# Kernel tuning notes

Hardware: AMD Instinct MI355X
Metric: run time of the kernel (lower is better)

Reference implementation:

```python
import jax, jax.numpy as jnp
import numpy as np

B, N, D, H, O, K, N_USER, C = 1, 4096, 64, 4, 64, 2, 4000, 2


def setup_inputs() -> dict:
    key = jax.random.key(0)
    ks = jax.random.split(key, 7)
    h = jax.random.normal(ks[0], (B, N, D), jnp.float32)
    # dense 0/1 adjacency per heterogeneous kind, with self-loops so no row is empty
    adj = jax.random.randint(ks[1], (K, B, N, N), 0, 2).astype(jnp.float32)
    hadj = jnp.maximum(adj, jnp.eye(N, dtype=jnp.float32))
    s = 1.0 / np.sqrt(D).astype(np.float32)
    w = jax.random.normal(ks[2], (K, H, D, O), jnp.float32) * s
    a_src = jax.random.normal(ks[3], (K, H, O, 1), jnp.float32) * (1.0 / np.sqrt(O).astype(np.float32))
    a_dst = jax.random.normal(ks[4], (K, H, O, 1), jnp.float32) * (1.0 / np.sqrt(O).astype(np.float32))
    fc_w = jax.random.normal(ks[5], (C, O * K), jnp.float32) * (1.0 / np.sqrt(O * K).astype(np.float32))
    fc_b = jnp.zeros((C,), jnp.float32)
    return {"h": h, "hadj": hadj, "w": w, "a_src": a_src, "a_dst": a_dst, "fc_w": fc_w, "fc_b": fc_b}


def _gat(h, adj, w_k, a_src_k, a_dst_k):
    # h: (B,N,D); adj: (B,N,N); w_k: (H,D,O); a_*: (H,O,1)
    h_prime = jnp.einsum('bnf,hfo->bhno', h, w_k)          # (B,H,N,O)
    t = jnp.tanh(h_prime)
    attn_src = jnp.einsum('bhno,hoi->bhni', t, a_src_k)    # (B,H,N,1)
    attn_dst = jnp.einsum('bhno,hoi->bhni', t, a_dst_k)    # (B,H,N,1)
    attn = attn_src + jnp.swapaxes(attn_dst, -1, -2)       # (B,H,N,N) broadcast add
    attn = jnp.where(attn >= 0, attn, 0.2 * attn)          # LeakyReLU(0.2)
    attn = jnp.where(adj[:, None] > 0, attn, -jnp.inf)     # dense mask
    attn = jax.nn.softmax(attn, axis=-1)                   # dropout is a no-op in eval
    out = jnp.einsum('bhnm,bhmo->bhno', attn, h_prime)     # (B,H,N,O)
    return out.mean(axis=1)                                # mean over heads -> (B,N,O)


def reference(h, hadj, w, a_src, a_dst, fc_w, fc_b):
    embs = []
    for k in range(K):  # small fixed loop over heterogeneous node kinds
        x = _gat(h, hadj[k], w[k], a_src[k], a_dst[k])
        embs.append(x[:, :N_USER])
    type_aware = jnp.concatenate(embs, axis=-1)            # (B, N_USER, K*O)
    logits = type_aware @ fc_w.T + fc_b                    # (B, N_USER, C)
    return jax.nn.log_softmax(logits, axis=-1)
```

## Files before the change

### kernel.cpp

```cpp
#include <hip/hip_runtime.h>
#include <math.h>

constexpr int KK = 2;
constexpr int HH = 4;
constexpr int NN = 4096;
constexpr int DD = 64;
constexpr int OO = 64;
constexpr int NU = 4000;
constexpr int CC = 2;
constexpr float LOG2E = 1.44269504088896340736f;

typedef float vf4 __attribute__((ext_vector_type(4)));
typedef float vf2 __attribute__((ext_vector_type(2)));

__device__ __forceinline__ float fexp2(float x) {
#if __has_builtin(__builtin_amdgcn_exp2f)
  return __builtin_amdgcn_exp2f(x);
#else
  return exp2f(x);
#endif
}
__device__ __forceinline__ float frcp(float x) {
#if __has_builtin(__builtin_amdgcn_rcpf)
  return __builtin_amdgcn_rcpf(x);
#else
  return 1.0f / x;
#endif
}
__device__ __forceinline__ float ftanh(float x) {
  float e = fexp2(x * (2.0f * LOG2E));
  return 1.0f - 2.0f * frcp(e + 1.0f);
}

__global__ __launch_bounds__(256) void gat_phase1(
    const float* __restrict__ hsrc, const float* __restrict__ w,
    const float* __restrict__ a_src, const float* __restrict__ a_dst,
    const float* __restrict__ fc_w,
    float* __restrict__ srcAA, float* __restrict__ Bp,
    float* __restrict__ B5p, float* __restrict__ g0p,
    float* __restrict__ g1p) {
  const int kh = blockIdx.y;
  const int k = kh >> 2;
  const int i0 = blockIdx.x * 64;
  const int tid = threadIdx.x;

  __shared__ float h_s[DD][68];
  __shared__ float w_s[DD][OO];
  __shared__ float part[4][64][17];

  {
    const vf4* wp = (const vf4*)(w + (size_t)kh * DD * OO);
    vf4* ws4 = (vf4*)w_s;
    for (int t = tid; t < DD * OO / 4; t += 256) ws4[t] = wp[t];
  }
  for (int t = tid; t < 1024; t += 256) {
    const int row = t >> 4;
    const int f4 = (t & 15) * 4;
    vf4 v = *(const vf4*)(hsrc + (size_t)(i0 + row) * DD + f4);
    h_s[f4 + 0][row] = v.x;
    h_s[f4 + 1][row] = v.y;
    h_s[f4 + 2][row] = v.z;
    h_s[f4 + 3][row] = v.w;
  }
  __syncthreads();

  const int og = tid & 15;
  const int rg = tid >> 4;
  const int o0 = og * 4;
  const int r0 = rg * 4;

  float hp[4][4];
#pragma unroll
  for (int j = 0; j < 4; ++j)
#pragma unroll
    for (int u = 0; u < 4; ++u) hp[j][u] = 0.0f;

#pragma unroll 8
  for (int f = 0; f < DD; ++f) {
    vf4 hv = *(const vf4*)&h_s[f][r0];
    vf4 wv = *(const vf4*)&w_s[f][o0];
    hp[0][0] = fmaf(hv.x, wv.x, hp[0][0]);
    hp[0][1] = fmaf(hv.x, wv.y, hp[0][1]);
    hp[0][2] = fmaf(hv.x, wv.z, hp[0][2]);
    hp[0][3] = fmaf(hv.x, wv.w, hp[0][3]);
    hp[1][0] = fmaf(hv.y, wv.x, hp[1][0]);
    hp[1][1] = fmaf(hv.y, wv.y, hp[1][1]);
    hp[1][2] = fmaf(hv.y, wv.z, hp[1][2]);
    hp[1][3] = fmaf(hv.y, wv.w, hp[1][3]);
    hp[2][0] = fmaf(hv.z, wv.x, hp[2][0]);
    hp[2][1] = fmaf(hv.z, wv.y, hp[2][1]);
    hp[2][2] = fmaf(hv.z, wv.z, hp[2][2]);
    hp[2][3] = fmaf(hv.z, wv.w, hp[2][3]);
    hp[3][0] = fmaf(hv.w, wv.x, hp[3][0]);
    hp[3][1] = fmaf(hv.w, wv.y, hp[3][1]);
    hp[3][2] = fmaf(hv.w, wv.z, hp[3][2]);
    hp[3][3] = fmaf(hv.w, wv.w, hp[3][3]);
  }

  float as[4], ad[4], f0[4], f1[4];
#pragma unroll
  for (int u = 0; u < 4; ++u) {
    as[u] = a_src[kh * OO + o0 + u];
    ad[u] = a_dst[kh * OO + o0 + u];
    f0[u] = fc_w[0 * (KK * OO) + k * OO + o0 + u];
    f1[u] = fc_w[1 * (KK * OO) + k * OO + o0 + u];
  }

#pragma unroll
  for (int j = 0; j < 4; ++j) {
    float sp = 0.0f, dp = 0.0f, g0 = 0.0f, g1 = 0.0f;
#pragma unroll
    for (int u = 0; u < 4; ++u) {
      float v = hp[j][u];
      float t = ftanh(v);
      sp = fmaf(t, as[u], sp);
      dp = fmaf(t, ad[u], dp);
      g0 = fmaf(v, f0[u], g0);
      g1 = fmaf(v, f1[u], g1);
    }
    part[0][r0 + j][og] = sp;
    part[1][r0 + j][og] = dp;
    part[2][r0 + j][og] = g0;
    part[3][r0 + j][og] = g1;
  }
  __syncthreads();

  {
    const int val = tid & 3;
    const int j2 = tid >> 2;
    const float* pr = &part[val][j2][0];
    vf4 s0 = *(const vf4*)(pr + 0);
    vf4 s1 = *(const vf4*)(pr + 4);
    vf4 s2 = *(const vf4*)(pr + 8);
    vf4 s3 = *(const vf4*)(pr + 12);
    vf4 t4 = s0 + s1 + s2 + s3;
    float sum = t4.x + t4.y + t4.z + t4.w;
    const size_t idx = (size_t)kh * NN + i0 + j2;
    if (val == 0) {
      float sp = sum * LOG2E;
      vf2 v = {fexp2(sp), fexp2(0.2f * sp)};
      *(vf2*)(srcAA + idx * 2) = v;
    } else if (val == 1) {
      float dp = sum * LOG2E;
      Bp[idx] = fexp2(dp);
      B5p[idx] = fexp2(0.2f * dp);
    } else if (val == 2) {
      g0p[idx] = sum;
    } else {
      g1p[idx] = sum;
    }
  }
}

__global__ __launch_bounds__(256) void gat_phase2(
    const float* __restrict__ adj, const float* __restrict__ srcAA,
    const float* __restrict__ Bp, const float* __restrict__ B5p,
    const float* __restrict__ g0p, const float* __restrict__ g1p,
    float* __restrict__ S) {
  const int k = blockIdx.y;
  const int r0 = blockIdx.x * 4;
  const int tid = threadIdx.x;
  const int wave = tid >> 6;
  const int lane = tid & 63;

  float A[4][4], A5[4][4];
#pragma unroll
  for (int h = 0; h < 4; ++h) {
    const float* base = srcAA + ((size_t)(k * HH + h) * NN + r0) * 2;
#pragma unroll
    for (int r = 0; r < 4; ++r) {
      A[r][h] = base[r * 2 + 0];
      A5[r][h] = base[r * 2 + 1];
    }
  }

  vf2 l2[4][4], a02[4][4], a12[4][4];
#pragma unroll
  for (int r = 0; r < 4; ++r)
#pragma unroll
    for (int h = 0; h < 4; ++h) {
      l2[r][h] = (vf2)(0.0f);
      a02[r][h] = (vf2)(0.0f);
      a12[r][h] = (vf2)(0.0f);
    }

  const float* adjk = adj + (size_t)k * NN * NN;
  const int jw = wave * 1024 + lane * 4;

#pragma unroll 1
  for (int t = 0; t < 4; ++t) {
    const int j = jw + t * 256;
    vf4 av[4];
#pragma unroll
    for (int r = 0; r < 4; ++r)
      av[r] = *(const vf4*)(adjk + (size_t)(r0 + r) * NN + j);
#pragma unroll
    for (int h = 0; h < 4; ++h) {
      const size_t pb = (size_t)(k * HH + h) * NN + j;
      vf4 b = *(const vf4*)(Bp + pb);
      vf4 b5 = *(const vf4*)(B5p + pb);
      vf4 g0 = *(const vf4*)(g0p + pb);
      vf4 g1 = *(const vf4*)(g1p + pb);
      vf2 blo = {b.x, b.y}, bhi = {b.z, b.w};
      vf2 b5lo = {b5.x, b5.y}, b5hi = {b5.z, b5.w};
      vf2 g0lo = {g0.x, g0.y}, g0hi = {g0.z, g0.w};
      vf2 g1lo = {g1.x, g1.y}, g1hi = {g1.z, g1.w};
#pragma unroll
      for (int r = 0; r < 4; ++r) {
        vf2 alo = {av[r].x, av[r].y}, ahi = {av[r].z, av[r].w};
        {
          vf2 e = __builtin_elementwise_max(blo * A[r][h], b5lo * A5[r][h]);
          vf2 pa = e * alo;
          l2[r][h] += pa;
          a02[r][h] = __builtin_elementwise_fma(pa, g0lo, a02[r][h]);
          a12[r][h] = __builtin_elementwise_fma(pa, g1lo, a12[r][h]);
        }
        {
          vf2 e = __builtin_elementwise_max(bhi * A[r][h], b5hi * A5[r][h]);
          vf2 pa = e * ahi;
          l2[r][h] += pa;
          a02[r][h] = __builtin_elementwise_fma(pa, g0hi, a02[r][h]);
          a12[r][h] = __builtin_elementwise_fma(pa, g1hi, a12[r][h]);
        }
      }
    }
  }

  float red[4][4][3];
#pragma unroll
  for (int r = 0; r < 4; ++r)
#pragma unroll
    for (int h = 0; h < 4; ++h) {
      float x0 = l2[r][h].x + l2[r][h].y;
      float x1 = a02[r][h].x + a02[r][h].y;
      float x2 = a12[r][h].x + a12[r][h].y;
#pragma unroll
      for (int off = 32; off > 0; off >>= 1) {
        x0 += __shfl_xor(x0, off, 64);
        x1 += __shfl_xor(x1, off, 64);
        x2 += __shfl_xor(x2, off, 64);
      }
      red[r][h][0] = x0;
      red[r][h][1] = x1;
      red[r][h][2] = x2;
    }

  __shared__ float sred[4][48];
  if (lane == 0) {
#pragma unroll
    for (int r = 0; r < 4; ++r)
#pragma unroll
      for (int h = 0; h < 4; ++h) {
#pragma unroll
        for (int c = 0; c < 3; ++c)
          sred[wave][(r * 4 + h) * 3 + c] = red[r][h][c];
      }
  }
  __syncthreads();
  if (tid < 8) {
    const int r = tid >> 1, c = tid & 1;
    float acc = 0.0f;
#pragma unroll
    for (int h = 0; h < 4; ++h) {
      const int vb = (r * 4 + h) * 3;
      float ls = sred[0][vb] + sred[1][vb] + sred[2][vb] + sred[3][vb];
      float ac = sred[0][vb + 1 + c] + sred[1][vb + 1 + c] +
                 sred[2][vb + 1 + c] + sred[3][vb + 1 + c];
      acc += ac / ls;
    }
    S[((size_t)k * NU + r0 + r) * CC + c] = 0.25f * acc;
  }
}

__global__ __launch_bounds__(256) void gat_phase3(
    const float* __restrict__ S, const float* __restrict__ fc_b,
    float* __restrict__ out) {
  const int i = blockIdx.x * 256 + threadIdx.x;
  if (i >= NU) return;
  float l0 = S[(size_t)i * CC + 0] + S[((size_t)NU + i) * CC + 0] + fc_b[0];
  float l1 = S[(size_t)i * CC + 1] + S[((size_t)NU + i) * CC + 1] + fc_b[1];
  float m = fmaxf(l0, l1);
  float lse = m + logf(expf(l0 - m) + expf(l1 - m));
  out[i * CC + 0] = l0 - lse;
  out[i * CC + 1] = l1 - lse;
}

extern "C" void kernel_launch(void* const* d_in, const int* in_sizes, int n_in,
                              void* d_out, int out_size, void* d_ws, size_t ws_size,
                              hipStream_t stream) {
  const float* hsrc  = (const float*)d_in[0];
  const float* hadj  = (const float*)d_in[1];
  const float* w     = (const float*)d_in[2];
  const float* a_src = (const float*)d_in[3];
  const float* a_dst = (const float*)d_in[4];
  const float* fc_w  = (const float*)d_in[5];
  const float* fc_b  = (const float*)d_in[6];
  float* out = (float*)d_out;

  char* ws = (char*)d_ws;
  float* srcAA = (float*)(ws + 0);
  float* Bp    = (float*)(ws + 262144);
  float* B5p   = (float*)(ws + 393216);
  float* g0p   = (float*)(ws + 524288);
  float* g1p   = (float*)(ws + 655360);
  float* S     = (float*)(ws + 786432);

  dim3 g1(NN / 64, KK * HH);
  gat_phase1<<<g1, 256, 0, stream>>>(hsrc, w, a_src, a_dst, fc_w,
                                     srcAA, Bp, B5p, g0p, g1p);
  dim3 g2(NU / 4, KK);
  gat_phase2<<<g2, 256, 0, stream>>>(hadj, srcAA, Bp, B5p, g0p, g1p, S);
  gat_phase3<<<(NU + 255) / 256, 256, 0, stream>>>(S, fc_b, out);
}
```

Before: 231.5 us.

## Prefetch adjacency and per-head tiles in phase2; shrink phase1 tile to 32 rows

```diff
diff --git a/kernel.cpp b/kernel.cpp
--- a/kernel.cpp
+++ b/kernel.cpp
@@ -41,43 +41,42 @@
     float* __restrict__ g1p) {
   const int kh = blockIdx.y;
   const int k = kh >> 2;
-  const int i0 = blockIdx.x * 64;
+  const int i0 = blockIdx.x * 32;
   const int tid = threadIdx.x;
 
-  __shared__ float h_s[DD][68];
   __shared__ float w_s[DD][OO];
-  __shared__ float part[4][64][17];
+  __shared__ float hs_un[DD * 36];
 
   {
     const vf4* wp = (const vf4*)(w + (size_t)kh * DD * OO);
     vf4* ws4 = (vf4*)w_s;
     for (int t = tid; t < DD * OO / 4; t += 256) ws4[t] = wp[t];
   }
-  for (int t = tid; t < 1024; t += 256) {
+  for (int t = tid; t < 512; t += 256) {
     const int row = t >> 4;
     const int f4 = (t & 15) * 4;
     vf4 v = *(const vf4*)(hsrc + (size_t)(i0 + row) * DD + f4);
-    h_s[f4 + 0][row] = v.x;
-    h_s[f4 + 1][row] = v.y;
-    h_s[f4 + 2][row] = v.z;
-    h_s[f4 + 3][row] = v.w;
+    hs_un[(f4 + 0) * 36 + row] = v.x;
+    hs_un[(f4 + 1) * 36 + row] = v.y;
+    hs_un[(f4 + 2) * 36 + row] = v.z;
+    hs_un[(f4 + 3) * 36 + row] = v.w;
   }
   __syncthreads();
 
   const int og = tid & 15;
   const int rg = tid >> 4;
   const int o0 = og * 4;
-  const int r0 = rg * 4;
-
-  float hp[4][4];
-#pragma unroll
-  for (int j = 0; j < 4; ++j)
+  const int r0 = rg * 2;
+
+  float hp[2][4];
+#pragma unroll
+  for (int j = 0; j < 2; ++j)
 #pragma unroll
     for (int u = 0; u < 4; ++u) hp[j][u] = 0.0f;
 
 #pragma unroll 8
   for (int f = 0; f < DD; ++f) {
-    vf4 hv = *(const vf4*)&h_s[f][r0];
+    vf2 hv = *(const vf2*)&hs_un[f * 36 + r0];
     vf4 wv = *(const vf4*)&w_s[f][o0];
     hp[0][0] = fmaf(hv.x, wv.x, hp[0][0]);
     hp[0][1] = fmaf(hv.x, wv.y, hp[0][1]);
@@ -87,14 +86,6 @@
     hp[1][1] = fmaf(hv.y, wv.y, hp[1][1]);
     hp[1][2] = fmaf(hv.y, wv.z, hp[1][2]);
     hp[1][3] = fmaf(hv.y, wv.w, hp[1][3]);
-    hp[2][0] = fmaf(hv.z, wv.x, hp[2][0]);
-    hp[2][1] = fmaf(hv.z, wv.y, hp[2][1]);
-    hp[2][2] = fmaf(hv.z, wv.z, hp[2][2]);
-    hp[2][3] = fmaf(hv.z, wv.w, hp[2][3]);
-    hp[3][0] = fmaf(hv.w, wv.x, hp[3][0]);
-    hp[3][1] = fmaf(hv.w, wv.y, hp[3][1]);
-    hp[3][2] = fmaf(hv.w, wv.z, hp[3][2]);
-    hp[3][3] = fmaf(hv.w, wv.w, hp[3][3]);
   }
 
   float as[4], ad[4], f0[4], f1[4];
@@ -106,8 +97,9 @@
     f1[u] = fc_w[1 * (KK * OO) + k * OO + o0 + u];
   }
 
-#pragma unroll
-  for (int j = 0; j < 4; ++j) {
+  float vals[2][4];
+#pragma unroll
+  for (int j = 0; j < 2; ++j) {
     float sp = 0.0f, dp = 0.0f, g0 = 0.0f, g1 = 0.0f;
 #pragma unroll
     for (int u = 0; u < 4; ++u) {
@@ -118,17 +110,25 @@
       g0 = fmaf(v, f0[u], g0);
       g1 = fmaf(v, f1[u], g1);
     }
-    part[0][r0 + j][og] = sp;
-    part[1][r0 + j][og] = dp;
-    part[2][r0 + j][og] = g0;
-    part[3][r0 + j][og] = g1;
+    vals[j][0] = sp;
+    vals[j][1] = dp;
+    vals[j][2] = g0;
+    vals[j][3] = g1;
   }
   __syncthreads();
 
-  {
+#pragma unroll
+  for (int j = 0; j < 2; ++j) {
+#pragma unroll
+    for (int v = 0; v < 4; ++v)
+      hs_un[(v * 32 + r0 + j) * 17 + og] = vals[j][v];
+  }
+  __syncthreads();
+
+  if (tid < 128) {
     const int val = tid & 3;
     const int j2 = tid >> 2;
-    const float* pr = &part[val][j2][0];
+    const float* pr = &hs_un[(val * 32 + j2) * 17];
     vf4 s0 = *(const vf4*)(pr + 0);
     vf4 s1 = *(const vf4*)(pr + 4);
     vf4 s2 = *(const vf4*)(pr + 8);
@@ -174,56 +174,64 @@
     }
   }
 
-  vf2 l2[4][4], a02[4][4], a12[4][4];
+  float l[4][4], a0[4][4], a1[4][4];
 #pragma unroll
   for (int r = 0; r < 4; ++r)
 #pragma unroll
     for (int h = 0; h < 4; ++h) {
-      l2[r][h] = (vf2)(0.0f);
-      a02[r][h] = (vf2)(0.0f);
-      a12[r][h] = (vf2)(0.0f);
+      l[r][h] = 0.0f;
+      a0[r][h] = 0.0f;
+      a1[r][h] = 0.0f;
     }
 
   const float* adjk = adj + (size_t)k * NN * NN;
   const int jw = wave * 1024 + lane * 4;
+
+  vf4 avc[4], avn[4];
+#pragma unroll
+  for (int r = 0; r < 4; ++r)
+    avc[r] = *(const vf4*)(adjk + (size_t)(r0 + r) * NN + jw);
 
 #pragma unroll 1
   for (int t = 0; t < 4; ++t) {
     const int j = jw + t * 256;
-    vf4 av[4];
-#pragma unroll
-    for (int r = 0; r < 4; ++r)
-      av[r] = *(const vf4*)(adjk + (size_t)(r0 + r) * NN + j);
+    if (t < 3) {
+#pragma unroll
+      for (int r = 0; r < 4; ++r)
+        avn[r] = *(const vf4*)(adjk + (size_t)(r0 + r) * NN + j + 256);
+    }
+    size_t pb = (size_t)(k * HH + 0) * NN + j;
+    vf4 bC = *(const vf4*)(Bp + pb);
+    vf4 b5C = *(const vf4*)(B5p + pb);
+    vf4 g0C = *(const vf4*)(g0p + pb);
+    vf4 g1C = *(const vf4*)(g1p + pb);
 #pragma unroll
     for (int h = 0; h < 4; ++h) {
-      const size_t pb = (size_t)(k * HH + h) * NN + j;
-      vf4 b = *(const vf4*)(Bp + pb);
-      vf4 b5 = *(const vf4*)(B5p + pb);
-      vf4 g0 = *(const vf4*)(g0p + pb);
-      vf4 g1 = *(const vf4*)(g1p + pb);
+      vf4 b = bC, b5 = b5C, g0 = g0C, g1 = g1C;
+      if (h < 3) {
+        size_t pn = (size_t)(k * HH + h + 1) * NN + j;
+        bC = *(const vf4*)(Bp + pn);
+        b5C = *(const vf4*)(B5p + pn);
+        g0C = *(const vf4*)(g0p + pn);
+        g1C = *(const vf4*)(g1p + pn);
+      }
       vf2 blo = {b.x, b.y}, bhi = {b.z, b.w};
       vf2 b5lo = {b5.x, b5.y}, b5hi = {b5.z, b5.w};
-      vf2 g0lo = {g0.x, g0.y}, g0hi = {g0.z, g0.w};
-      vf2 g1lo = {g1.x, g1.y}, g1hi = {g1.z, g1.w};
 #pragma unroll
       for (int r = 0; r < 4; ++r) {
-        vf2 alo = {av[r].x, av[r].y}, ahi = {av[r].z, av[r].w};
-        {
-          vf2 e = __builtin_elementwise_max(blo * A[r][h], b5lo * A5[r][h]);
-          vf2 pa = e * alo;
-          l2[r][h] += pa;
-          a02[r][h] = __builtin_elementwise_fma(pa, g0lo, a02[r][h]);
-          a12[r][h] = __builtin_elementwise_fma(pa, g1lo, a12[r][h]);
-        }
-        {
-          vf2 e = __builtin_elementwise_max(bhi * A[r][h], b5hi * A5[r][h]);
-          vf2 pa = e * ahi;
-          l2[r][h] += pa;
-          a02[r][h] = __builtin_elementwise_fma(pa, g0hi, a02[r][h]);
-          a12[r][h] = __builtin_elementwise_fma(pa, g1hi, a12[r][h]);
-        }
+        vf2 elo = __builtin_elementwise_max(blo * A[r][h], b5lo * A5[r][h]);
+        vf2 ehi = __builtin_elementwise_max(bhi * A[r][h], b5hi * A5[r][h]);
+        float p0 = elo.x * avc[r].x;
+        float p1 = elo.y * avc[r].y;
+        float p2 = ehi.x * avc[r].z;
+        float p3 = ehi.y * avc[r].w;
+        l[r][h] += (p0 + p1) + (p2 + p3);
+        a0[r][h] = fmaf(p0, g0.x, fmaf(p1, g0.y, fmaf(p2, g0.z, fmaf(p3, g0.w, a0[r][h]))));
+        a1[r][h] = fmaf(p0, g1.x, fmaf(p1, g1.y, fmaf(p2, g1.z, fmaf(p3, g1.w, a1[r][h]))));
       }
     }
+#pragma unroll
+    for (int r = 0; r < 4; ++r) avc[r] = avn[r];
   }
 
   float red[4][4][3];
@@ -231,9 +239,7 @@
   for (int r = 0; r < 4; ++r)
 #pragma unroll
     for (int h = 0; h < 4; ++h) {
-      float x0 = l2[r][h].x + l2[r][h].y;
-      float x1 = a02[r][h].x + a02[r][h].y;
-      float x2 = a12[r][h].x + a12[r][h].y;
+      float x0 = l[r][h], x1 = a0[r][h], x2 = a1[r][h];
 #pragma unroll
       for (int off = 32; off > 0; off >>= 1) {
         x0 += __shfl_xor(x0, off, 64);
@@ -305,7 +311,7 @@
   float* g1p   = (float*)(ws + 655360);
   float* S     = (float*)(ws + 786432);
 
-  dim3 g1(NN / 64, KK * HH);
+  dim3 g1(NN / 32, KK * HH);
   gat_phase1<<<g1, 256, 0, stream>>>(hsrc, w, a_src, a_dst, fc_w,
                                      srcAA, Bp, B5p, g0p, g1p);
   dim3 g2(NU / 4, KK);
```

Result: no change. 235.6 us (+1.8%).
